# Kernel optimization log

Measured on AMD Instinct MI355X. Metric: run time of the kernel, lower is better.

The kernel has to match this reference:

```python
import jax, jax.numpy as jnp
import numpy as np

B, C, O, H, W = 8, 64, 64, 128, 128


def conv3x3(x, w, b):
    # x: [B,Cin,H,W], w: [Cout,Cin,3,3], stride 1, padding 1
    y = jax.lax.conv_general_dilated(
        x, w, window_strides=(1, 1), padding=((1, 1), (1, 1)),
        dimension_numbers=("NCHW", "OIHW", "NCHW"))
    return y + b[None, :, None, None]


def setup_inputs() -> dict:
    key = jax.random.key(0)
    ks = jax.random.split(key, 6)
    fan = C * 9
    x = jax.random.normal(ks[0], (B, C, H, W), dtype=jnp.float32)
    w_main = jax.random.normal(ks[1], (O, C, 3, 3), dtype=jnp.float32) / np.sqrt(fan)
    # small offset weights keep sampled locations near the regular grid (realistic post-training regime)
    w_offset = jax.random.normal(ks[2], (18, C, 3, 3), dtype=jnp.float32) * 0.05 / np.sqrt(fan)
    b_offset = jnp.zeros((18,), dtype=jnp.float32)
    w_mask = jax.random.normal(ks[3], (9, C, 3, 3), dtype=jnp.float32) / np.sqrt(fan)
    b_mask = jnp.zeros((9,), dtype=jnp.float32)
    return {"x": x, "w_main": w_main, "w_offset": w_offset,
            "b_offset": b_offset, "w_mask": w_mask, "b_mask": b_mask}


def deform_conv2d(x, w_main, offset, mask):
    # torchvision.ops.deform_conv2d: kernel 3x3, stride 1, pad 1, dilation 1, no bias
    Bb, Cc, Hh, Ww = x.shape
    Oo = w_main.shape[0]
    off = offset.reshape(Bb, 9, 2, Hh, Ww)
    dy, dx = off[:, :, 0], off[:, :, 1]            # [B,9,H,W]; pairs ordered (y,x), k row-major
    k = jnp.arange(9)
    kh = (k // 3 - 1).astype(x.dtype)              # kernel row offset in {-1,0,1}
    kw = (k % 3 - 1).astype(x.dtype)
    iy = jnp.arange(Hh, dtype=x.dtype)
    ix = jnp.arange(Ww, dtype=x.dtype)
    # sampling positions p = p0 + p_k + delta_p
    py = dy + iy[None, None, :, None] + kh[None, :, None, None]
    px = dx + ix[None, None, None, :] + kw[None, :, None, None]

    y0 = jnp.floor(py)
    x0 = jnp.floor(px)
    ly = py - y0
    lx = px - x0
    y0i = y0.astype(jnp.int32)
    x0i = x0.astype(jnp.int32)
    y1i = y0i + 1
    x1i = x0i + 1

    bidx = jnp.arange(Bb)[:, None, None, None]

    def corner(yi, xi, wgt):
        # zero-padding semantics: out-of-bounds neighbors contribute 0
        valid = (yi >= 0) & (yi < Hh) & (xi >= 0) & (xi < Ww)
        v = x[bidx, :, jnp.clip(yi, 0, Hh - 1), jnp.clip(xi, 0, Ww - 1)]  # [B,9,H,W,C]
        return v * (wgt * valid)[..., None]

    samp = (corner(y0i, x0i, (1 - ly) * (1 - lx))
            + corner(y0i, x1i, (1 - ly) * lx)
            + corner(y1i, x0i, ly * (1 - lx))
            + corner(y1i, x1i, ly * lx))
    samp = samp * mask[..., None]                  # modulation mask (dcn v2)
    # contract sampled patches with weights: [B,9,H,W,C] x [O,C,9] -> [B,O,H,W]
    return jnp.einsum("bkhwc,ock->bohw", samp, w_main.reshape(Oo, Cc, 9))


def reference(x, w_main, w_offset, b_offset, w_mask, b_mask):
    offset = conv3x3(x, w_offset, b_offset)                 # [B,18,H,W]
    mask = jax.nn.sigmoid(conv3x3(x, w_mask, b_mask))       # [B,9,H,W]
    return deform_conv2d(x, w_main, offset, mask)
```

## Files before the change

### kernel.cpp

```cpp
#include <hip/hip_runtime.h>
#include <math.h>

#define BB 8
#define CC 64
#define OO 64
#define HH 128
#define WW 128
#define HW (HH*WW)
#define NPIX (BB*HW)

typedef __bf16 bf16x8 __attribute__((ext_vector_type(8)));
typedef float floatx4 __attribute__((ext_vector_type(4)));
typedef unsigned short ushort_t;

#define XT_BYTES  16777216
#define OM_BYTES  14680064
#define WT_BYTES  73728

__device__ __forceinline__ unsigned short f2b(float f) {
    unsigned u = __float_as_uint(f);
    u += 0x7fffu + ((u >> 16) & 1u);
    return (unsigned short)(u >> 16);
}

__device__ __forceinline__ void unpack8(uint4 q, float* f) {
    f[0] = __uint_as_float(q.x << 16); f[1] = __uint_as_float(q.x & 0xffff0000u);
    f[2] = __uint_as_float(q.y << 16); f[3] = __uint_as_float(q.y & 0xffff0000u);
    f[4] = __uint_as_float(q.z << 16); f[5] = __uint_as_float(q.z & 0xffff0000u);
    f[6] = __uint_as_float(q.w << 16); f[7] = __uint_as_float(q.w & 0xffff0000u);
}

__global__ __launch_bounds__(256) void transpose_kernel(
    const float* __restrict__ x, ushort_t* __restrict__ xt)
{
    __shared__ float tile[64][33];
    int bh = blockIdx.x;
    int w0 = blockIdx.y * 32;
    int b  = bh >> 7;
    int h  = bh & 127;
    int t  = threadIdx.x;
    int tx = t & 31;
    int ty = t >> 5;

    #pragma unroll
    for (int j = 0; j < 8; ++j) {
        int c = ty * 8 + j;
        tile[c][tx] = x[(((size_t)(b*CC + c))*HH + h)*WW + (w0 + tx)];
    }
    __syncthreads();
    #pragma unroll
    for (int j = 0; j < 4; ++j) {
        int w  = ty + 8*j;
        int cp = tx;
        unsigned u = (unsigned)f2b(tile[2*cp][w]) |
                     ((unsigned)f2b(tile[2*cp+1][w]) << 16);
        *(unsigned*)(xt + (((size_t)(b*HH + h))*WW + (w0 + w))*CC + 2*cp) = u;
    }
}

__global__ __launch_bounds__(256) void repack_kernel(
    const float* __restrict__ wm, const float* __restrict__ woff,
    const float* __restrict__ wmask, ushort_t* __restrict__ wt,
    ushort_t* __restrict__ wb)
{
    int i = blockIdx.x * 256 + threadIdx.x;
    if (i < 36864) {
        int o = i / 576, k = i % 576, tap = k >> 6, c = k & 63;
        wt[i] = f2b(wm[o*576 + c*9 + tap]);
    }
    int j = i - 36864;
    if (j >= 0 && j < 18432) {
        int o = j / 576, k = j % 576, tap = k >> 6, c = k & 63;
        float v = 0.f;
        if (o < 18)      v = woff[o*576 + c*9 + tap];
        else if (o < 27) v = wmask[(o-18)*576 + c*9 + tap];
        wb[j] = f2b(v);
    }
}

__global__ __launch_bounds__(256) void conv27_kernel(
    const ushort_t* __restrict__ xt, const ushort_t* __restrict__ wb,
    const float* __restrict__ boff, const float* __restrict__ bmsk,
    float* __restrict__ om)
{
    __shared__ ushort_t win[18*18*72];
    int bid = blockIdx.x;
    int b  = bid >> 6;
    int th = (bid >> 3) & 7;
    int tw = bid & 7;
    int h0 = th * 16, w0 = tw * 16;
    int t = threadIdx.x;

    for (int idx = t; idx < 18*18*8; idx += 256) {
        int r   = idx / 144;
        int rem = idx - r*144;
        int col = rem >> 3;
        int ch  = (rem & 7) << 3;
        int y = h0 + r - 1, x = w0 + col - 1;
        uint4 val = make_uint4(0,0,0,0);
        if ((unsigned)y < (unsigned)HH && (unsigned)x < (unsigned)WW)
            val = *(const uint4*)(xt + ((((size_t)b*HH + y)*WW + x) << 6) + ch);
        *(uint4*)(win + (r*18 + col)*72 + ch) = val;
    }
    __syncthreads();

    int lane = t & 63, wv = t >> 6;
    int n = lane & 15, quad = lane >> 4;
    const ushort_t* wb0 = wb + n*576;
    const ushort_t* wb1 = wb + (16 + n)*576;

    floatx4 acc0[4], acc1[4];
    #pragma unroll
    for (int mt = 0; mt < 4; ++mt) {
        acc0[mt] = (floatx4){0.f,0.f,0.f,0.f};
        acc1[mt] = (floatx4){0.f,0.f,0.f,0.f};
    }

    #pragma unroll
    for (int s = 0; s < 18; ++s) {
        int tap  = s >> 1;
        int tr   = tap / 3, tc = tap % 3;
        int coff = (s & 1)*32 + quad*8;
        int kk = tap*64 + coff;
        bf16x8 b0 = *(const bf16x8*)(wb0 + kk);
        bf16x8 b1 = *(const bf16x8*)(wb1 + kk);
        #pragma unroll
        for (int mt = 0; mt < 4; ++mt) {
            int ty = wv*4 + mt;
            bf16x8 a = *(const bf16x8*)(win + ((ty + tr)*18 + (n + tc))*72 + coff);
            acc0[mt] = __builtin_amdgcn_mfma_f32_16x16x32_bf16(a, b0, acc0[mt], 0, 0, 0);
            acc1[mt] = __builtin_amdgcn_mfma_f32_16x16x32_bf16(a, b1, acc1[mt], 0, 0, 0);
        }
    }

    #pragma unroll
    for (int mt = 0; mt < 4; ++mt) {
        int ty = wv*4 + mt;
        #pragma unroll
        for (int r = 0; r < 4; ++r) {
            int tx = quad*4 + r;
            size_t p = ((size_t)(b*HH + h0 + ty))*WW + (w0 + tx);
            float* dst = om + p*28;
            dst[n] = acc0[mt][r] + boff[n];
            int o1 = 16 + n;
            if (o1 < 18) {
                dst[o1] = acc1[mt][r] + boff[o1];
            } else if (o1 < 27) {
                float z = acc1[mt][r] + bmsk[o1 - 18];
                dst[o1] = 1.f / (1.f + expf(-z));
            } else if (o1 == 27) {
                dst[27] = 0.f;
            }
        }
    }
}

__global__ __launch_bounds__(256) void deform_kernel(
    const ushort_t* __restrict__ xt, const float* __restrict__ om,
    const ushort_t* __restrict__ wt, float* __restrict__ out)
{
    __shared__ ushort_t samp[2*128*72];

    int t = threadIdx.x;
    int lane = t & 63, wv = t >> 6;
    int p0 = blockIdx.x * 128;
    int b  = p0 >> 14;

    int pa = t >> 1, hf = t & 1;
    int gp = p0 + pa;
    int h_a = (gp >> 7) & 127, w_a = gp & 127;
    const float* omp = om + (size_t)gp * 28;
    const ushort_t* xbase = xt + ((size_t)b << 20);

    int n = lane & 15, quad = lane >> 4;
    floatx4 acc[8];
    #pragma unroll
    for (int i = 0; i < 8; ++i) acc[i] = (floatx4){0.f,0.f,0.f,0.f};
    const ushort_t* wrow = wt + (wv*16 + n)*576;

    for (int k = 0; k < 9; ++k) {
        ushort_t* sb = samp + (k & 1) * (128*72);

        int kr = k / 3, kc = k - kr*3;
        float dy = omp[2*k], dx = omp[2*k + 1], m = omp[18 + k];
        float py = (float)(h_a + kr - 1) + dy;
        float px = (float)(w_a + kc - 1) + dx;
        float y0f = floorf(py), x0f = floorf(px);
        float ly = py - y0f, lx = px - x0f;
        int y0 = (int)y0f, x0 = (int)x0f, y1 = y0 + 1, x1 = x0 + 1;
        float vy0 = ((unsigned)y0 < (unsigned)HH) ? 1.f : 0.f;
        float vy1 = ((unsigned)y1 < (unsigned)HH) ? 1.f : 0.f;
        float vx0 = ((unsigned)x0 < (unsigned)WW) ? 1.f : 0.f;
        float vx1 = ((unsigned)x1 < (unsigned)WW) ? 1.f : 0.f;

        float cw[4] = { (1.f-ly)*(1.f-lx)*vy0*vx0*m,
                        (1.f-ly)*lx      *vy0*vx1*m,
                        ly*(1.f-lx)      *vy1*vx0*m,
                        ly*lx            *vy1*vx1*m };
        int ys[4] = { y0, y0, y1, y1 };
        int xs[4] = { x0, x1, x0, x1 };

        float v[32];
        #pragma unroll
        for (int i = 0; i < 32; ++i) v[i] = 0.f;

        #pragma unroll
        for (int cn = 0; cn < 4; ++cn) {
            int yc = min(max(ys[cn], 0), HH-1);
            int xc = min(max(xs[cn], 0), WW-1);
            const uint4* cp = (const uint4*)(xbase + (((yc << 7) + xc) << 6) + hf*32);
            uint4 q0 = cp[0], q1 = cp[1], q2 = cp[2], q3 = cp[3];
            float f[32];
            unpack8(q0, f); unpack8(q1, f + 8);
            unpack8(q2, f + 16); unpack8(q3, f + 24);
            float wg = cw[cn];
            #pragma unroll
            for (int j = 0; j < 32; ++j) v[j] += wg * f[j];
        }

        __syncthreads();
        {
            unsigned uu[16];
            #pragma unroll
            for (int j = 0; j < 16; ++j)
                uu[j] = (unsigned)f2b(v[2*j]) | ((unsigned)f2b(v[2*j+1]) << 16);
            uint4* dst = (uint4*)(sb + pa*72 + hf*32);
            dst[0] = make_uint4(uu[0],  uu[1],  uu[2],  uu[3]);
            dst[1] = make_uint4(uu[4],  uu[5],  uu[6],  uu[7]);
            dst[2] = make_uint4(uu[8],  uu[9],  uu[10], uu[11]);
            dst[3] = make_uint4(uu[12], uu[13], uu[14], uu[15]);
        }
        __syncthreads();

        #pragma unroll
        for (int half = 0; half < 2; ++half) {
            bf16x8 bfrag = *(const bf16x8*)(wrow + k*64 + half*32 + quad*8);
            #pragma unroll
            for (int mt = 0; mt < 8; ++mt) {
                bf16x8 afrag = *(const bf16x8*)(sb + (mt*16 + n)*72 + half*32 + quad*8);
                acc[mt] = __builtin_amdgcn_mfma_f32_16x16x32_bf16(afrag, bfrag, acc[mt], 0, 0, 0);
            }
        }
    }

    int hw0 = p0 & 16383;
    float* op = out + ((size_t)b*OO + (wv*16 + n))*HW;
    #pragma unroll
    for (int mt = 0; mt < 8; ++mt) {
        float4 st = make_float4(acc[mt][0], acc[mt][1], acc[mt][2], acc[mt][3]);
        *(float4*)(op + hw0 + mt*16 + quad*4) = st;
    }
}

extern "C" void kernel_launch(void* const* d_in, const int* in_sizes, int n_in,
                              void* d_out, int out_size, void* d_ws, size_t ws_size,
                              hipStream_t stream)
{
    const float* x      = (const float*)d_in[0];
    const float* w_main = (const float*)d_in[1];
    const float* w_off  = (const float*)d_in[2];
    const float* b_off  = (const float*)d_in[3];
    const float* w_msk  = (const float*)d_in[4];
    const float* b_msk  = (const float*)d_in[5];
    float* out = (float*)d_out;

    unsigned char* ws = (unsigned char*)d_ws;
    ushort_t* xt = (ushort_t*)ws;
    float*    om = (float*)(ws + XT_BYTES);
    ushort_t* wt = (ushort_t*)(ws + XT_BYTES + OM_BYTES);
    ushort_t* wb = (ushort_t*)(ws + XT_BYTES + OM_BYTES + WT_BYTES);

    dim3 tgrid(BB*HH, WW/32);
    transpose_kernel<<<tgrid, 256, 0, stream>>>(x, xt);

    repack_kernel<<<(36864 + 18432 + 255)/256, 256, 0, stream>>>(
        w_main, w_off, w_msk, wt, wb);

    conv27_kernel<<<NPIX/256, 256, 0, stream>>>(xt, wb, b_off, b_msk, om);

    deform_kernel<<<NPIX/128, 256, 0, stream>>>(xt, om, wt, out);
}
```

Before: 183.1 us.

## Tile deform kernel into 8x8 spatial blocks with 4 threads per pixel

The deformable conv kernel now assigns each block an 8x8 spatial tile of 64 pixels instead of a 128-pixel row strip, with four threads per pixel each gathering 16 channels. The aim is better cache locality for the bilinear gathers and more blocks for occupancy. It also prefetches the next tap's offsets and mask, and moves the barrier to the end of the loop. The trade-off is half the MFMA work per block, so weight fragments are reloaded more often relative to compute.

```diff
diff --git a/kernel.cpp b/kernel.cpp
--- a/kernel.cpp
+++ b/kernel.cpp
@@ -159,30 +159,37 @@
     const ushort_t* __restrict__ xt, const float* __restrict__ om,
     const ushort_t* __restrict__ wt, float* __restrict__ out)
 {
-    __shared__ ushort_t samp[2*128*72];
+    __shared__ ushort_t samp[2*64*72];
 
     int t = threadIdx.x;
     int lane = t & 63, wv = t >> 6;
-    int p0 = blockIdx.x * 128;
-    int b  = p0 >> 14;
-
-    int pa = t >> 1, hf = t & 1;
-    int gp = p0 + pa;
-    int h_a = (gp >> 7) & 127, w_a = gp & 127;
-    const float* omp = om + (size_t)gp * 28;
+    int bid = blockIdx.x;
+    int b  = bid >> 8;
+    int th = (bid >> 4) & 15;
+    int tw = bid & 15;
+    int h0 = th * 8, w0 = tw * 8;
+
+    int pa = t >> 2, cg = t & 3;
+    int ph = pa >> 3, pw = pa & 7;
+    int h_a = h0 + ph, w_a = w0 + pw;
+    const float* omp = om + (((size_t)(b*HH + h_a))*WW + w_a) * 28;
     const ushort_t* xbase = xt + ((size_t)b << 20);
 
     int n = lane & 15, quad = lane >> 4;
-    floatx4 acc[8];
-    #pragma unroll
-    for (int i = 0; i < 8; ++i) acc[i] = (floatx4){0.f,0.f,0.f,0.f};
+    floatx4 acc[4];
+    #pragma unroll
+    for (int i = 0; i < 4; ++i) acc[i] = (floatx4){0.f,0.f,0.f,0.f};
     const ushort_t* wrow = wt + (wv*16 + n)*576;
 
+    float dy = omp[0], dx = omp[1], m = omp[18];
+
     for (int k = 0; k < 9; ++k) {
-        ushort_t* sb = samp + (k & 1) * (128*72);
+        ushort_t* sb = samp + (k & 1) * (64*72);
+
+        float dy_n = 0.f, dx_n = 0.f, m_n = 0.f;
+        if (k < 8) { dy_n = omp[2*k + 2]; dx_n = omp[2*k + 3]; m_n = omp[19 + k]; }
 
         int kr = k / 3, kc = k - kr*3;
-        float dy = omp[2*k], dx = omp[2*k + 1], m = omp[18 + k];
         float py = (float)(h_a + kr - 1) + dy;
         float px = (float)(w_a + kc - 1) + dx;
         float y0f = floorf(py), x0f = floorf(px);
@@ -200,35 +207,33 @@
         int ys[4] = { y0, y0, y1, y1 };
         int xs[4] = { x0, x1, x0, x1 };
 
-        float v[32];
-        #pragma unroll
-        for (int i = 0; i < 32; ++i) v[i] = 0.f;
+        dy = dy_n; dx = dx_n; m = m_n;
+
+        float v[16];
+        #pragma unroll
+        for (int i = 0; i < 16; ++i) v[i] = 0.f;
 
         #pragma unroll
         for (int cn = 0; cn < 4; ++cn) {
             int yc = min(max(ys[cn], 0), HH-1);
             int xc = min(max(xs[cn], 0), WW-1);
-            const uint4* cp = (const uint4*)(xbase + (((yc << 7) + xc) << 6) + hf*32);
-            uint4 q0 = cp[0], q1 = cp[1], q2 = cp[2], q3 = cp[3];
-            float f[32];
+            const uint4* cp = (const uint4*)(xbase + (((yc << 7) + xc) << 6) + cg*16);
+            uint4 q0 = cp[0], q1 = cp[1];
+            float f[16];
             unpack8(q0, f); unpack8(q1, f + 8);
-            unpack8(q2, f + 16); unpack8(q3, f + 24);
             float wg = cw[cn];
             #pragma unroll
-            for (int j = 0; j < 32; ++j) v[j] += wg * f[j];
-        }
-
-        __syncthreads();
+            for (int j = 0; j < 16; ++j) v[j] += wg * f[j];
+        }
+
         {
-            unsigned uu[16];
+            unsigned uu[8];
             #pragma unroll
-            for (int j = 0; j < 16; ++j)
+            for (int j = 0; j < 8; ++j)
                 uu[j] = (unsigned)f2b(v[2*j]) | ((unsigned)f2b(v[2*j+1]) << 16);
-            uint4* dst = (uint4*)(sb + pa*72 + hf*32);
-            dst[0] = make_uint4(uu[0],  uu[1],  uu[2],  uu[3]);
-            dst[1] = make_uint4(uu[4],  uu[5],  uu[6],  uu[7]);
-            dst[2] = make_uint4(uu[8],  uu[9],  uu[10], uu[11]);
-            dst[3] = make_uint4(uu[12], uu[13], uu[14], uu[15]);
+            uint4* dst = (uint4*)(sb + pa*72 + cg*16);
+            dst[0] = make_uint4(uu[0], uu[1], uu[2], uu[3]);
+            dst[1] = make_uint4(uu[4], uu[5], uu[6], uu[7]);
         }
         __syncthreads();
 
@@ -236,19 +241,21 @@
         for (int half = 0; half < 2; ++half) {
             bf16x8 bfrag = *(const bf16x8*)(wrow + k*64 + half*32 + quad*8);
             #pragma unroll
-            for (int mt = 0; mt < 8; ++mt) {
+            for (int mt = 0; mt < 4; ++mt) {
                 bf16x8 afrag = *(const bf16x8*)(sb + (mt*16 + n)*72 + half*32 + quad*8);
                 acc[mt] = __builtin_amdgcn_mfma_f32_16x16x32_bf16(afrag, bfrag, acc[mt], 0, 0, 0);
             }
         }
-    }
-
-    int hw0 = p0 & 16383;
+        __syncthreads();
+    }
+
     float* op = out + ((size_t)b*OO + (wv*16 + n))*HW;
     #pragma unroll
-    for (int mt = 0; mt < 8; ++mt) {
+    for (int mt = 0; mt < 4; ++mt) {
+        int row = h0 + mt*2 + (quad >> 1);
+        int col = w0 + (quad & 1)*4;
         float4 st = make_float4(acc[mt][0], acc[mt][1], acc[mt][2], acc[mt][3]);
-        *(float4*)(op + hw0 + mt*16 + quad*4) = st;
+        *(float4*)(op + row*WW + col) = st;
     }
 }
 
@@ -278,5 +285,5 @@
 
     conv27_kernel<<<NPIX/256, 256, 0, stream>>>(xt, wb, b_off, b_msk, om);
 
-    deform_kernel<<<NPIX/128, 256, 0, stream>>>(xt, om, wt, out);
-}
+    deform_kernel<<<NPIX/64, 256, 0, stream>>>(xt, om, wt, out);
+}
```

Result: faster. 162.9 us (-11.0%).
